# Optimization experiments

Hardware: AMD Instinct MI355X
Metric: run time of the kernel (lower is better)

The kernel has to match this reference:

```python
import jax, jax.numpy as jnp
import numpy as np
from jax import lax

# db5 (Daubechies-10) reconstruction lowpass filter, same values as pywt.Wavelet('db5').rec_lo
REC_LO = jnp.array([
    0.160102397974125,
    0.6038292697974729,
    0.7243085284385744,
    0.13842814590110342,
    -0.24229488706619015,
    -0.03224486958502952,
    0.07757149384006515,
    -0.006241490213011705,
    -0.012580751999015526,
    0.003335725285001549,
], dtype=jnp.float32)
DEC_LO = REC_LO[::-1]  # decomposition lowpass = reversed rec_lo
F = 10  # db5 filter length


def setup_inputs() -> dict:
    key = jax.random.key(0)
    x = jax.random.normal(key, (64, 128, 4096), dtype=jnp.float32)
    return {"x": x}


def reference(x) -> jnp.ndarray:
    # x: (B, C, L) -> flatten(1,2) -> (B, N) with N = C*L
    B, C, L = x.shape
    sig = x.reshape(B, 1, C * L)  # NCH layout, single channel

    # ---- DWT (db5, symmetric mode), lowpass branch only (cD is discarded upstream) ----
    # pywt equivalence: cA = np.convolve(pad(x, F-1, 'symmetric'), dec_lo, 'valid')[1::2]
    # np.convolve with dec_lo == correlation with rec_lo; offset-1 stride-2 downsampling
    ext = jnp.pad(sig, ((0, 0), (0, 0), (F - 1, F - 1)), mode="symmetric")
    k_dec = REC_LO.reshape(1, 1, F)
    cA = lax.conv_general_dilated(
        ext[:, :, 1:], k_dec,
        window_strides=(2,), padding=[(0, 0)],
        dimension_numbers=("NCH", "OIH", "NCH"),
    )  # (B, 1, (N+F-1)//2)

    # ---- IDWT from cA only: ya = pywt.idwt(cA, None, 'db5', 'smooth') ----
    # upsample by 2 (length 2*Nc-1), full-convolve with rec_lo, trim F-2 from each side
    # => transposed conv: lhs_dilation=2, correlation kernel = reversed rec_lo, pad (1,1)
    k_rec = DEC_LO.reshape(1, 1, F)
    ya = lax.conv_general_dilated(
        cA, k_rec,
        window_strides=(1,), padding=[(1, 1)], lhs_dilation=(2,),
        dimension_numbers=("NCH", "OIH", "NCH"),
    )  # (B, 1, 2*Nc - F + 2) -- matches torch .unsqueeze(1) output layout
    return ya
```

## Files before the change

kernel.cpp:

```cpp
#include <hip/hip_runtime.h>
#include <stdint.h>


#define L_SIG 524288
#define TILE  2048
#define HALO  16
#define SMEM_N (TILE + 2 * HALO)

typedef float f4 __attribute__((ext_vector_type(4)));

typedef __attribute__((address_space(3))) uint32_t lds_u32_t;
typedef const __attribute__((address_space(1))) uint32_t glb_u32_t;

__device__ __forceinline__ void stage16(const float* g, float* l) {
    __builtin_amdgcn_global_load_lds((glb_u32_t*)g, (lds_u32_t*)l, 16, 0, 0);
}

constexpr float RL[10] = {
    0.160102397974125f,   0.6038292697974729f,  0.7243085284385744f,
    0.13842814590110342f, -0.24229488706619015f, -0.03224486958502952f,
    0.07757149384006515f, -0.006241490213011705f, -0.012580751999015526f,
    0.003335725285001549f};

struct Coef { float we[18]; float wo[18]; };

constexpr Coef make_coef() {
    Coef c{};
    for (int d = 0; d < 18; ++d) {
        float se = 0.f, so = 0.f;
        for (int j = 0; j < 5; ++j) {
            int i = d - 2 * j;
            if (i >= 0 && i < 10) {
                se += RL[8 - 2 * j] * RL[i];
                so += RL[9 - 2 * j] * RL[i];
            }
        }
        c.we[d] = se;
        c.wo[d] = so;
    }
    return c;
}

constexpr Coef CF = make_coef();

__global__ __launch_bounds__(256)
void wavelet_fused_kernel(const float* __restrict__ x, float* __restrict__ out) {
    __shared__ float s[SMEM_N];

    const int batch = blockIdx.y;
    const int p0    = blockIdx.x * TILE;
    const float* xb = x   + (size_t)batch * L_SIG;
    float*       ob = out + (size_t)batch * L_SIG;
    const int t = threadIdx.x;

    const bool edge = (blockIdx.x == 0) || (blockIdx.x == gridDim.x - 1);

    if (edge) {
        for (int i = t; i < SMEM_N; i += 256) {
            int k  = p0 - HALO + i;
            int km = (k < 0) ? (-1 - k) : ((k >= L_SIG) ? (2 * L_SIG - 1 - k) : k);
            s[i] = xb[km];
        }
    } else {
        const float* src = xb + p0 - HALO;
        stage16(src + 4 * t,        s + 4 * t);
        stage16(src + 1024 + 4 * t, s + 1024 + 4 * t);
        if (t < 8)
            stage16(src + 2048 + 4 * t, s + 2048 + 4 * t);
    }
    __syncthreads();

#pragma unroll
    for (int h = 0; h < 2; ++h) {
        const int q = 4 * t + 1024 * h;

        float v[20];
        const f4* sp = (const f4*)(s + q + 8);
#pragma unroll
        for (int r = 0; r < 5; ++r) {
            f4 f = sp[r];
            v[4 * r + 0] = f[0];
            v[4 * r + 1] = f[1];
            v[4 * r + 2] = f[2];
            v[4 * r + 3] = f[3];
        }

        float o0 = 0.f, o1 = 0.f, o2 = 0.f, o3 = 0.f;
#pragma unroll
        for (int d = 0; d < 18; ++d) {
            o0 += CF.we[d] * v[d];
            o1 += CF.wo[d] * v[d];
            o2 += CF.we[d] * v[d + 2];
            o3 += CF.wo[d] * v[d + 2];
        }

        f4 o = {o0, o1, o2, o3};
        __builtin_nontemporal_store(o, (f4*)(ob + p0 + q));
    }
}

extern "C" void kernel_launch(void* const* d_in, const int* in_sizes, int n_in,
                              void* d_out, int out_size, void* d_ws, size_t ws_size,
                              hipStream_t stream) {
    const float* x = (const float*)d_in[0];
    float* out     = (float*)d_out;

    const int B = in_sizes[0] / L_SIG;
    dim3 grid(L_SIG / TILE, B);
    wavelet_fused_kernel<<<grid, 256, 0, stream>>>(x, out);
}
```

Measured before the change: 228.3 us.

## Persistent blocks with double-buffered LDS tile prefetch

Replaces the one-tile-per-block grid with a fixed grid of 2048 blocks, each processing 8 consecutive tiles. The next tile is staged into a second LDS buffer with async global_load_lds while the current tile is computed, so load latency overlaps compute and store. It removes block launch overhead and exposed load latency, at the cost of less parallelism per tile, a barrier per iteration, and a hardcoded batch count of 64 (the grid no longer comes from the input size).

```diff
diff --git a/kernel.cpp b/kernel.cpp
--- a/kernel.cpp
+++ b/kernel.cpp
@@ -5,7 +5,10 @@
 #define L_SIG 524288
 #define TILE  2048
 #define HALO  16
-#define SMEM_N (TILE + 2 * HALO)
+#define TPB_F (TILE + 2 * HALO)
+#define TILES_PER_BATCH (L_SIG / TILE)
+#define NBLOCKS 2048
+#define TILES_PER_BLOCK 8
 
 typedef float f4 __attribute__((ext_vector_type(4)));
 
@@ -45,57 +48,74 @@
 
 __global__ __launch_bounds__(256)
 void wavelet_fused_kernel(const float* __restrict__ x, float* __restrict__ out) {
-    __shared__ float s[SMEM_N];
+    __shared__ float s[2][TPB_F];
+    const int t    = threadIdx.x;
+    const int tau0 = blockIdx.x * TILES_PER_BLOCK;
 
-    const int batch = blockIdx.y;
-    const int p0    = blockIdx.x * TILE;
-    const float* xb = x   + (size_t)batch * L_SIG;
-    float*       ob = out + (size_t)batch * L_SIG;
-    const int t = threadIdx.x;
+    auto stage = [&](int tau, float* buf) {
+        const int    tb = tau & (TILES_PER_BATCH - 1);
+        const float* xb = x + ((size_t)(tau >> 8) << 19);
+        const int    p0 = tb * TILE;
+        if (tb == 0 || tb == TILES_PER_BATCH - 1) {
+            for (int i = t; i < TPB_F; i += 256) {
+                int k  = p0 - HALO + i;
+                int km = (k < 0) ? (-1 - k) : ((k >= L_SIG) ? (2 * L_SIG - 1 - k) : k);
+                buf[i] = xb[km];
+            }
+        } else {
+            const float* src = xb + p0 - HALO;
+            stage16(src + 4 * t,        buf + 4 * t);
+            stage16(src + 1024 + 4 * t, buf + 1024 + 4 * t);
+            if (t < 8)
+                stage16(src + 2048 + 4 * t, buf + 2048 + 4 * t);
+        }
+    };
 
-    const bool edge = (blockIdx.x == 0) || (blockIdx.x == gridDim.x - 1);
-
-    if (edge) {
-        for (int i = t; i < SMEM_N; i += 256) {
-            int k  = p0 - HALO + i;
-            int km = (k < 0) ? (-1 - k) : ((k >= L_SIG) ? (2 * L_SIG - 1 - k) : k);
-            s[i] = xb[km];
-        }
-    } else {
-        const float* src = xb + p0 - HALO;
-        stage16(src + 4 * t,        s + 4 * t);
-        stage16(src + 1024 + 4 * t, s + 1024 + 4 * t);
-        if (t < 8)
-            stage16(src + 2048 + 4 * t, s + 2048 + 4 * t);
-    }
+    stage(tau0, s[0]);
     __syncthreads();
 
+    int cur = 0;
+#pragma unroll 1
+    for (int it = 0; it < TILES_PER_BLOCK; ++it) {
+        const int tau = tau0 + it;
+
+        if (it + 1 < TILES_PER_BLOCK)
+            stage(tau + 1, &s[cur ^ 1][0]);
+
+        const float* sb = &s[cur][0];
+        float* ob = out + ((size_t)(tau >> 8) << 19)
+                        + (size_t)(tau & (TILES_PER_BATCH - 1)) * TILE;
+
 #pragma unroll
-    for (int h = 0; h < 2; ++h) {
-        const int q = 4 * t + 1024 * h;
+        for (int h = 0; h < 2; ++h) {
+            const int q = 4 * t + 1024 * h;
 
-        float v[20];
-        const f4* sp = (const f4*)(s + q + 8);
+            float v[20];
+            const f4* sp = (const f4*)(sb + q + 8);
 #pragma unroll
-        for (int r = 0; r < 5; ++r) {
-            f4 f = sp[r];
-            v[4 * r + 0] = f[0];
-            v[4 * r + 1] = f[1];
-            v[4 * r + 2] = f[2];
-            v[4 * r + 3] = f[3];
+            for (int r = 0; r < 5; ++r) {
+                f4 f = sp[r];
+                v[4 * r + 0] = f[0];
+                v[4 * r + 1] = f[1];
+                v[4 * r + 2] = f[2];
+                v[4 * r + 3] = f[3];
+            }
+
+            float o0 = 0.f, o1 = 0.f, o2 = 0.f, o3 = 0.f;
+#pragma unroll
+            for (int d = 0; d < 18; ++d) {
+                o0 += CF.we[d] * v[d];
+                o1 += CF.wo[d] * v[d];
+                o2 += CF.we[d] * v[d + 2];
+                o3 += CF.wo[d] * v[d + 2];
+            }
+
+            f4 o = {o0, o1, o2, o3};
+            __builtin_nontemporal_store(o, (f4*)(ob + q));
         }
 
-        float o0 = 0.f, o1 = 0.f, o2 = 0.f, o3 = 0.f;
-#pragma unroll
-        for (int d = 0; d < 18; ++d) {
-            o0 += CF.we[d] * v[d];
-            o1 += CF.wo[d] * v[d];
-            o2 += CF.we[d] * v[d + 2];
-            o3 += CF.wo[d] * v[d + 2];
-        }
-
-        f4 o = {o0, o1, o2, o3};
-        __builtin_nontemporal_store(o, (f4*)(ob + p0 + q));
+        __syncthreads();
+        cur ^= 1;
     }
 }
 
@@ -104,8 +124,5 @@
                               hipStream_t stream) {
     const float* x = (const float*)d_in[0];
     float* out     = (float*)d_out;
-
-    const int B = in_sizes[0] / L_SIG;
-    dim3 grid(L_SIG / TILE, B);
-    wavelet_fused_kernel<<<grid, 256, 0, stream>>>(x, out);
+    wavelet_fused_kernel<<<NBLOCKS, 256, 0, stream>>>(x, out);
 }
```

Measured after the change: 236.7 us. 3.7% more time.
